# Performance work log

Hardware: AMD Instinct MI355X
Metric: run time of the kernel (lower is better)

Reference implementation:

```python
import jax, jax.numpy as jnp
import numpy as np

K_VALUES = (2, 4, 8)  # sorted k_values from init


def setup_inputs() -> dict:
    key = jax.random.key(0)
    ks = jax.random.split(key, 6)
    B, T, D, H = 16, 2048, 512, 64
    nk = len(K_VALUES)
    # columns: (E, Pt, eta, phi) -- E,Pt positive, eta in [-3,3], phi in [-pi,pi]
    u = jax.random.uniform(ks[0], (B, T, 4), jnp.float32)
    tokens_cont = u * jnp.array([100.0, 50.0, 6.0, 6.2832], jnp.float32) + jnp.array([1.0, 1.0, -3.0, -3.1416], jnp.float32)
    lengths = jax.random.randint(ks[1], (B,), T // 2, T + 1)
    mask = jnp.arange(T)[None, :] < lengths[:, None]  # [B,T] True=valid
    W1 = jax.random.normal(ks[2], (nk, H), jnp.float32) / np.sqrt(nk).astype(np.float32)
    b1 = jax.random.normal(ks[3], (H,), jnp.float32) * 0.01
    W2 = jax.random.normal(ks[4], (H, D), jnp.float32) / np.sqrt(H).astype(np.float32)
    b2 = jax.random.normal(ks[5], (D,), jnp.float32) * 0.01
    return dict(tokens_cont=tokens_cont, mask=mask, W1=W1, b1=b1, W2=W2, b2=b2)


def reference(tokens_cont, mask, W1, b1, W2, b2):
    B, T, _ = tokens_cont.shape
    E, Pt, eta, phi = (tokens_cont[..., i] for i in range(4))
    px = Pt * jnp.cos(phi)
    py = Pt * jnp.sin(phi)
    pz = Pt * jnp.sinh(jnp.clip(eta, -20.0, 20.0))
    P = jnp.stack([E, px, py, pz], axis=-1)  # [B,T,4] four-momentum
    metric = jnp.array([1.0, -1.0, -1.0, -1.0], P.dtype)
    # Lorentz dot: E_i E_j - px_i px_j - py_i py_j - pz_i pz_j -> [B,T,T]
    dot = jnp.einsum('btc,bsc->bts', P * metric, P)
    dot = jnp.where(mask[:, None, :], dot, -jnp.inf)  # exclude padding friends
    max_k = min(max(K_VALUES), T)
    _, topk_idx = jax.lax.top_k(dot, max_k)  # [B,T,max_k]
    Pf = P[jnp.arange(B)[:, None, None], topk_idx]  # gather friends [B,T,max_k,4]
    cum = jnp.cumsum(Pf, axis=2)  # prefix sums over sorted friends
    masses = []
    maskf = mask.astype(P.dtype)
    for k in K_VALUES:
        ps = cum[:, :, min(k, max_k) - 1, :]  # [B,T,4] summed 4-momentum of top-k group
        m2 = ps[..., 0] ** 2 - jnp.sum(ps[..., 1:] ** 2, axis=-1)
        m2 = jnp.maximum(m2, 0.0) * maskf
        masses.append(jnp.sqrt(m2 + 1e-8))
    mass = jnp.stack(masses, axis=-1)  # [B,T,n_k]
    h = jax.nn.gelu(mass @ W1 + b1, approximate=False)  # torch GELU = exact erf
    return h @ W2 + b2  # [B,T,model_dim]
```

## Files before the change

### kernel.cpp

```cpp
#include <hip/hip_runtime.h>
#include <hip/hip_bf16.h>
#include <math.h>

#define NB 16
#define NT 2048
#define ND 512
#define NH 64

typedef __attribute__((ext_vector_type(8))) short short8;
typedef __attribute__((ext_vector_type(4))) float float4v;

__device__ __forceinline__ bool mask_is_bytes(const int* m) {
    return m[0] == 0x01010101;
}
__device__ __forceinline__ bool mask_at(const int* m, bool bytes, int i) {
    if (bytes) return ((const unsigned char*)m)[i] != 0;
    return m[i] != 0;
}

__device__ __forceinline__ float dot4(float4 a, float4 p) {
    float d = a.x * p.x;
    d = __builtin_fmaf(a.y, p.y, d);
    d = __builtin_fmaf(a.z, p.z, d);
    d = __builtin_fmaf(a.w, p.w, d);
    return d;
}

__device__ __forceinline__ unsigned short f2bf(float x) {
    unsigned int u = __float_as_uint(x);
    u += 0x7fffu + ((u >> 16) & 1u);
    return (unsigned short)(u >> 16);
}

#define INS8(V0,V1,V2,V3,V4,V5,V6,V7,D)                          \
    {                                                            \
        float n0 = fmaxf(V0, D);                                 \
        float n1 = __builtin_amdgcn_fmed3f(D, V0, V1);           \
        float n2 = __builtin_amdgcn_fmed3f(D, V1, V2);           \
        float n3 = __builtin_amdgcn_fmed3f(D, V2, V3);           \
        float n4 = __builtin_amdgcn_fmed3f(D, V3, V4);           \
        float n5 = __builtin_amdgcn_fmed3f(D, V4, V5);           \
        float n6 = __builtin_amdgcn_fmed3f(D, V5, V6);           \
        float n7 = __builtin_amdgcn_fmed3f(D, V6, V7);           \
        V0 = n0; V1 = n1; V2 = n2; V3 = n3;                      \
        V4 = n4; V5 = n5; V6 = n6; V7 = n7;                      \
    }

__global__ void __launch_bounds__(256) w2t_kernel(
        const float* __restrict__ W2, unsigned short* __restrict__ W2t) {
    int i = blockIdx.x * 256 + threadIdx.x;
    int n = i & (ND - 1), k = i >> 9;
    W2t[n * NH + k] = f2bf(W2[k * ND + n]);
}

#define VT(w2, j, l)  scratch[((w2) * 8 + (j)) * 128 + (l)]
#define PS(w2, c, l)  scratch[((w2) * 12 + (c)) * 128 + (l)]

__global__ void __launch_bounds__(512) fused_topk_mass_mlp_kernel(
        const float* __restrict__ tok,
        const int* __restrict__ mask,
        const float* __restrict__ W1,
        const float* __restrict__ b1,
        const unsigned short* __restrict__ W2t,
        const float* __restrict__ b2,
        float* __restrict__ out) {
    __shared__ float Plds[NT * 4];
    __shared__ float scratch[8 * 12 * 128];
    __shared__ unsigned short hs[64][88];
    __shared__ float mass_s[3][128];
    __shared__ int wcnt[8];

    const int b    = blockIdx.y;
    const int t0   = blockIdx.x * 128;
    const int tid  = threadIdx.x;
    const int lane = tid & 63;
    const int w    = tid >> 6;
    const bool mb  = mask_is_bytes(mask);

    const bool blockValid = mask_at(mask, mb, b * NT + t0);

    if (blockValid) {
        int cnt = 0;
#pragma unroll
        for (int it = 0; it < 4; ++it) {
            int i = tid + it * 512;
            float4 tv = ((const float4*)tok)[b * NT + i];
            bool m = mask_at(mask, mb, b * NT + i);
            float E = tv.x, Pt = tv.y, eta = tv.z, phi = tv.w;
            float px = Pt * cosf(phi);
            float py = Pt * sinf(phi);
            float pz = Pt * sinhf(fminf(fmaxf(eta, -20.f), 20.f));
            float4 pv = m ? make_float4(E, px, py, pz)
                          : make_float4(-1e30f, 0.f, 0.f, 0.f);
            *(float4*)&Plds[i * 4] = pv;
            cnt += (int)__popcll(__ballot(m));
        }
        if (lane == 0) wcnt[w] = cnt;
        __syncthreads();

        int L = 0;
#pragma unroll
        for (int j = 0; j < 8; ++j) L += wcnt[j];
        const int C    = (L + 7) >> 3;
        const int sBeg = w * C;
        const int sEnd = min(sBeg + C, L);

        float4 ptA = *(const float4*)&Plds[(t0 + lane) * 4];
        float4 ptB = *(const float4*)&Plds[(t0 + 64 + lane) * 4];
        float4 aA  = make_float4(ptA.x, -ptA.y, -ptA.z, -ptA.w);
        float4 aB  = make_float4(ptB.x, -ptB.y, -ptB.z, -ptB.w);

        const float NEGBIG = -3.402823466e38f;
        float A0 = NEGBIG, A1 = NEGBIG, A2 = NEGBIG, A3 = NEGBIG;
        float A4 = NEGBIG, A5 = NEGBIG, A6 = NEGBIG, A7 = NEGBIG;
        float B0 = NEGBIG, B1 = NEGBIG, B2 = NEGBIG, B3 = NEGBIG;
        float B4 = NEGBIG, B5 = NEGBIG, B6 = NEGBIG, B7 = NEGBIG;

#pragma unroll 4
        for (int s = sBeg; s < sEnd; ++s) {
            float4 ps = *(const float4*)&Plds[s * 4];
            float dA = dot4(aA, ps);
            float dB = dot4(aB, ps);
            INS8(A0, A1, A2, A3, A4, A5, A6, A7, dA);
            INS8(B0, B1, B2, B3, B4, B5, B6, B7, dB);
        }
        VT(w, 0, lane) = A0; VT(w, 1, lane) = A1;
        VT(w, 2, lane) = A2; VT(w, 3, lane) = A3;
        VT(w, 4, lane) = A4; VT(w, 5, lane) = A5;
        VT(w, 6, lane) = A6; VT(w, 7, lane) = A7;
        VT(w, 0, 64 + lane) = B0; VT(w, 1, 64 + lane) = B1;
        VT(w, 2, 64 + lane) = B2; VT(w, 3, 64 + lane) = B3;
        VT(w, 4, 64 + lane) = B4; VT(w, 5, 64 + lane) = B5;
        VT(w, 6, 64 + lane) = B6; VT(w, 7, 64 + lane) = B7;
        __syncthreads();

        float mA0 = NEGBIG, mA1 = NEGBIG, mA2 = NEGBIG, mA3 = NEGBIG;
        float mA4 = NEGBIG, mA5 = NEGBIG, mA6 = NEGBIG, mA7 = NEGBIG;
        float mB0 = NEGBIG, mB1 = NEGBIG, mB2 = NEGBIG, mB3 = NEGBIG;
        float mB4 = NEGBIG, mB5 = NEGBIG, mB6 = NEGBIG, mB7 = NEGBIG;
#pragma unroll
        for (int w2 = 0; w2 < 8; ++w2) {
#pragma unroll
            for (int j = 0; j < 8; ++j) {
                float dA = VT(w2, j, lane);
                float dB = VT(w2, j, 64 + lane);
                INS8(mA0, mA1, mA2, mA3, mA4, mA5, mA6, mA7, dA);
                INS8(mB0, mB1, mB2, mB3, mB4, mB5, mB6, mB7, dB);
            }
        }
        const float th2A = mA1, th4A = mA3, th8A = mA7;
        const float th2B = mB1, th4B = mB3, th8B = mB7;
        __syncthreads();

        float a2x = 0.f, a2y = 0.f, a2z = 0.f, a2w = 0.f;
        float a4x = 0.f, a4y = 0.f, a4z = 0.f, a4w = 0.f;
        float a8x = 0.f, a8y = 0.f, a8z = 0.f, a8w = 0.f;
        float b2x = 0.f, b2y = 0.f, b2z = 0.f, b2w = 0.f;
        float b4x = 0.f, b4y = 0.f, b4z = 0.f, b4w = 0.f;
        float b8x = 0.f, b8y = 0.f, b8z = 0.f, b8w = 0.f;
#pragma unroll 4
        for (int s = sBeg; s < sEnd; ++s) {
            float4 ps = *(const float4*)&Plds[s * 4];
            float dA = dot4(aA, ps);
            float dB = dot4(aB, ps);
            if (dA >= th8A) {
                a8x += ps.x; a8y += ps.y; a8z += ps.z; a8w += ps.w;
                if (dA >= th4A) {
                    a4x += ps.x; a4y += ps.y; a4z += ps.z; a4w += ps.w;
                    if (dA >= th2A) {
                        a2x += ps.x; a2y += ps.y; a2z += ps.z; a2w += ps.w;
                    }
                }
            }
            if (dB >= th8B) {
                b8x += ps.x; b8y += ps.y; b8z += ps.z; b8w += ps.w;
                if (dB >= th4B) {
                    b4x += ps.x; b4y += ps.y; b4z += ps.z; b4w += ps.w;
                    if (dB >= th2B) {
                        b2x += ps.x; b2y += ps.y; b2z += ps.z; b2w += ps.w;
                    }
                }
            }
        }
        PS(w, 0, lane) = a2x;  PS(w, 1, lane) = a2y;
        PS(w, 2, lane) = a2z;  PS(w, 3, lane) = a2w;
        PS(w, 4, lane) = a4x;  PS(w, 5, lane) = a4y;
        PS(w, 6, lane) = a4z;  PS(w, 7, lane) = a4w;
        PS(w, 8, lane) = a8x;  PS(w, 9, lane) = a8y;
        PS(w, 10, lane) = a8z; PS(w, 11, lane) = a8w;
        PS(w, 0, 64 + lane) = b2x;  PS(w, 1, 64 + lane) = b2y;
        PS(w, 2, 64 + lane) = b2z;  PS(w, 3, 64 + lane) = b2w;
        PS(w, 4, 64 + lane) = b4x;  PS(w, 5, 64 + lane) = b4y;
        PS(w, 6, 64 + lane) = b4z;  PS(w, 7, 64 + lane) = b4w;
        PS(w, 8, 64 + lane) = b8x;  PS(w, 9, 64 + lane) = b8y;
        PS(w, 10, 64 + lane) = b8z; PS(w, 11, 64 + lane) = b8w;
        __syncthreads();

        if (w < 2) {
            const int tl = w * 64 + lane;
            float tot[12];
#pragma unroll
            for (int c = 0; c < 12; ++c) {
                float acc = 0.f;
#pragma unroll
                for (int w2 = 0; w2 < 8; ++w2) acc += PS(w2, c, tl);
                tot[c] = acc;
            }
            const bool maskt = (t0 + tl) < L;
            const float MZ = sqrtf(1e-8f);
            auto massf = [&](float sx, float sy, float sz, float sw) -> float {
                float q = sx * sx;
                q = __builtin_fmaf(-sy, sy, q);
                q = __builtin_fmaf(-sz, sz, q);
                q = __builtin_fmaf(-sw, sw, q);
                q = fmaxf(q, 0.f);
                return sqrtf(q + 1e-8f);
            };
            mass_s[0][tl] = maskt ? massf(tot[0], tot[1], tot[2], tot[3]) : MZ;
            mass_s[1][tl] = maskt ? massf(tot[4], tot[5], tot[6], tot[7]) : MZ;
            mass_s[2][tl] = maskt ? massf(tot[8], tot[9], tot[10], tot[11]) : MZ;
        }
    } else {
        if (tid < 128) {
            const float MZ = sqrtf(1e-8f);
            mass_s[0][tid] = MZ;
            mass_s[1][tid] = MZ;
            mass_s[2][tid] = MZ;
        }
    }
    __syncthreads();

    const int col   = lane & 15;
    const int quad  = lane >> 4;
    const int mhalf = w >> 2;
    const int nBase = (w & 3) * 128;

#pragma unroll
    for (int half = 0; half < 2; ++half) {
        {
            const int tt = lane;
            const int hr = w;
            float q0 = mass_s[0][half * 64 + tt];
            float q1 = mass_s[1][half * 64 + tt];
            float q2 = mass_s[2][half * 64 + tt];
            unsigned short hv[8];
#pragma unroll
            for (int j = 0; j < 8; ++j) {
                int hh = hr * 8 + j;
                float pre = b1[hh];
                pre = __builtin_fmaf(q0, W1[hh], pre);
                pre = __builtin_fmaf(q1, W1[NH + hh], pre);
                pre = __builtin_fmaf(q2, W1[2 * NH + hh], pre);
                float g = 0.5f * pre * (1.0f + erff(pre * 0.70710678118654752f));
                hv[j] = f2bf(g);
            }
            *(short8*)&hs[tt][hr * 8] = *(const short8*)hv;
        }
        __syncthreads();

        short8 afrag[2][2];
#pragma unroll
        for (int mt = 0; mt < 2; ++mt)
#pragma unroll
            for (int ks = 0; ks < 2; ++ks)
                afrag[mt][ks] = *(const short8*)&hs[mhalf * 32 + mt * 16 + col][ks * 32 + quad * 8];

        float4v acc[2][8];
#pragma unroll
        for (int mt = 0; mt < 2; ++mt)
#pragma unroll
            for (int nt = 0; nt < 8; ++nt)
                acc[mt][nt] = (float4v)(0.f);

#pragma unroll
        for (int nt = 0; nt < 8; ++nt) {
            const unsigned short* wp = W2t + (nBase + nt * 16 + col) * NH + quad * 8;
            short8 bf0 = *(const short8*)(wp);
            short8 bf1 = *(const short8*)(wp + 32);
            acc[0][nt] = __builtin_amdgcn_mfma_f32_16x16x32_bf16(afrag[0][0], bf0, acc[0][nt], 0, 0, 0);
            acc[1][nt] = __builtin_amdgcn_mfma_f32_16x16x32_bf16(afrag[1][0], bf0, acc[1][nt], 0, 0, 0);
            acc[0][nt] = __builtin_amdgcn_mfma_f32_16x16x32_bf16(afrag[0][1], bf1, acc[0][nt], 0, 0, 0);
            acc[1][nt] = __builtin_amdgcn_mfma_f32_16x16x32_bf16(afrag[1][1], bf1, acc[1][nt], 0, 0, 0);
        }

#pragma unroll
        for (int nt = 0; nt < 8; ++nt) {
            float bias = b2[nBase + nt * 16 + col];
#pragma unroll
            for (int mt = 0; mt < 2; ++mt) {
                int mRow = b * NT + t0 + half * 64 + mhalf * 32 + mt * 16 + quad * 4;
                size_t base = (size_t)mRow * ND + nBase + nt * 16 + col;
#pragma unroll
                for (int r = 0; r < 4; ++r) {
                    out[base + (size_t)r * ND] = acc[mt][nt][r] + bias;
                }
            }
        }
        __syncthreads();
    }
}

extern "C" void kernel_launch(void* const* d_in, const int* in_sizes, int n_in,
                              void* d_out, int out_size, void* d_ws, size_t ws_size,
                              hipStream_t stream) {
    const float* tok  = (const float*)d_in[0];
    const int*   mask = (const int*)d_in[1];
    const float* W1   = (const float*)d_in[2];
    const float* b1   = (const float*)d_in[3];
    const float* W2   = (const float*)d_in[4];
    const float* b2   = (const float*)d_in[5];
    float*       out  = (float*)d_out;

    unsigned short* W2t = (unsigned short*)d_ws;

    w2t_kernel<<<dim3(ND * NH / 256), dim3(256), 0, stream>>>(W2, W2t);

    dim3 gB(NT / 128, NB);
    fused_topk_mass_mlp_kernel<<<gB, dim3(512), 0, stream>>>(
        tok, mask, W1, b1, W2t, b2, out);
}
```

Baseline: 148.7 us.

## Double block to 1024 threads, skip top-8 inserts via wave ballot, single-pass MLP

Raises the fused kernel to 16 waves per block so each wave scans half as many candidate friends. The 16 partial top-8 lists are merged, and the partial momentum sums are reduced in two steps through the same scratch buffer. The expensive 8-wide insertion network is now skipped whenever no lane in the wave has a candidate beating its current 8th-best. The MLP epilogue runs once over all 128 rows instead of two halves. Register pressure from launch_bounds(1024) may cause spills, and the larger scratch and hs arrays use more LDS.

```diff
diff --git a/kernel.cpp b/kernel.cpp
--- a/kernel.cpp
+++ b/kernel.cpp
@@ -56,7 +56,7 @@
 #define VT(w2, j, l)  scratch[((w2) * 8 + (j)) * 128 + (l)]
 #define PS(w2, c, l)  scratch[((w2) * 12 + (c)) * 128 + (l)]
 
-__global__ void __launch_bounds__(512) fused_topk_mass_mlp_kernel(
+__global__ void __launch_bounds__(1024, 4) fused_topk_mass_mlp_kernel(
         const float* __restrict__ tok,
         const int* __restrict__ mask,
         const float* __restrict__ W1,
@@ -65,10 +65,10 @@
         const float* __restrict__ b2,
         float* __restrict__ out) {
     __shared__ float Plds[NT * 4];
-    __shared__ float scratch[8 * 12 * 128];
-    __shared__ unsigned short hs[64][88];
+    __shared__ float scratch[16 * 8 * 128];
+    __shared__ unsigned short hs[128][88];
     __shared__ float mass_s[3][128];
-    __shared__ int wcnt[8];
+    __shared__ int wcnt[16];
 
     const int b    = blockIdx.y;
     const int t0   = blockIdx.x * 128;
@@ -82,8 +82,8 @@
     if (blockValid) {
         int cnt = 0;
 #pragma unroll
-        for (int it = 0; it < 4; ++it) {
-            int i = tid + it * 512;
+        for (int it = 0; it < 2; ++it) {
+            int i = tid + it * 1024;
             float4 tv = ((const float4*)tok)[b * NT + i];
             bool m = mask_at(mask, mb, b * NT + i);
             float E = tv.x, Pt = tv.y, eta = tv.z, phi = tv.w;
@@ -100,8 +100,8 @@
 
         int L = 0;
 #pragma unroll
-        for (int j = 0; j < 8; ++j) L += wcnt[j];
-        const int C    = (L + 7) >> 3;
+        for (int j = 0; j < 16; ++j) L += wcnt[j];
+        const int C    = (L + 15) >> 4;
         const int sBeg = w * C;
         const int sEnd = min(sBeg + C, L);
 
@@ -116,13 +116,14 @@
         float B0 = NEGBIG, B1 = NEGBIG, B2 = NEGBIG, B3 = NEGBIG;
         float B4 = NEGBIG, B5 = NEGBIG, B6 = NEGBIG, B7 = NEGBIG;
 
-#pragma unroll 4
         for (int s = sBeg; s < sEnd; ++s) {
             float4 ps = *(const float4*)&Plds[s * 4];
             float dA = dot4(aA, ps);
             float dB = dot4(aB, ps);
-            INS8(A0, A1, A2, A3, A4, A5, A6, A7, dA);
-            INS8(B0, B1, B2, B3, B4, B5, B6, B7, dB);
+            if (__ballot((dA > A7) || (dB > B7))) {
+                INS8(A0, A1, A2, A3, A4, A5, A6, A7, dA);
+                INS8(B0, B1, B2, B3, B4, B5, B6, B7, dB);
+            }
         }
         VT(w, 0, lane) = A0; VT(w, 1, lane) = A1;
         VT(w, 2, lane) = A2; VT(w, 3, lane) = A3;
@@ -139,7 +140,7 @@
         float mB0 = NEGBIG, mB1 = NEGBIG, mB2 = NEGBIG, mB3 = NEGBIG;
         float mB4 = NEGBIG, mB5 = NEGBIG, mB6 = NEGBIG, mB7 = NEGBIG;
 #pragma unroll
-        for (int w2 = 0; w2 < 8; ++w2) {
+        for (int w2 = 0; w2 < 16; ++w2) {
 #pragma unroll
             for (int j = 0; j < 8; ++j) {
                 float dA = VT(w2, j, lane);
@@ -155,10 +156,9 @@
         float a2x = 0.f, a2y = 0.f, a2z = 0.f, a2w = 0.f;
         float a4x = 0.f, a4y = 0.f, a4z = 0.f, a4w = 0.f;
         float a8x = 0.f, a8y = 0.f, a8z = 0.f, a8w = 0.f;
-        float b2x = 0.f, b2y = 0.f, b2z = 0.f, b2w = 0.f;
-        float b4x = 0.f, b4y = 0.f, b4z = 0.f, b4w = 0.f;
-        float b8x = 0.f, b8y = 0.f, b8z = 0.f, b8w = 0.f;
-#pragma unroll 4
+        float c2x = 0.f, c2y = 0.f, c2z = 0.f, c2w = 0.f;
+        float c4x = 0.f, c4y = 0.f, c4z = 0.f, c4w = 0.f;
+        float c8x = 0.f, c8y = 0.f, c8z = 0.f, c8w = 0.f;
         for (int s = sBeg; s < sEnd; ++s) {
             float4 ps = *(const float4*)&Plds[s * 4];
             float dA = dot4(aA, ps);
@@ -173,27 +173,46 @@
                 }
             }
             if (dB >= th8B) {
-                b8x += ps.x; b8y += ps.y; b8z += ps.z; b8w += ps.w;
+                c8x += ps.x; c8y += ps.y; c8z += ps.z; c8w += ps.w;
                 if (dB >= th4B) {
-                    b4x += ps.x; b4y += ps.y; b4z += ps.z; b4w += ps.w;
+                    c4x += ps.x; c4y += ps.y; c4z += ps.z; c4w += ps.w;
                     if (dB >= th2B) {
-                        b2x += ps.x; b2y += ps.y; b2z += ps.z; b2w += ps.w;
+                        c2x += ps.x; c2y += ps.y; c2z += ps.z; c2w += ps.w;
                     }
                 }
             }
         }
-        PS(w, 0, lane) = a2x;  PS(w, 1, lane) = a2y;
-        PS(w, 2, lane) = a2z;  PS(w, 3, lane) = a2w;
-        PS(w, 4, lane) = a4x;  PS(w, 5, lane) = a4y;
-        PS(w, 6, lane) = a4z;  PS(w, 7, lane) = a4w;
-        PS(w, 8, lane) = a8x;  PS(w, 9, lane) = a8y;
-        PS(w, 10, lane) = a8z; PS(w, 11, lane) = a8w;
-        PS(w, 0, 64 + lane) = b2x;  PS(w, 1, 64 + lane) = b2y;
-        PS(w, 2, 64 + lane) = b2z;  PS(w, 3, 64 + lane) = b2w;
-        PS(w, 4, 64 + lane) = b4x;  PS(w, 5, 64 + lane) = b4y;
-        PS(w, 6, 64 + lane) = b4z;  PS(w, 7, 64 + lane) = b4w;
-        PS(w, 8, 64 + lane) = b8x;  PS(w, 9, 64 + lane) = b8y;
-        PS(w, 10, 64 + lane) = b8z; PS(w, 11, 64 + lane) = b8w;
+
+        if (w >= 8) {
+            const int ws = w - 8;
+            PS(ws, 0, lane) = a2x;  PS(ws, 1, lane) = a2y;
+            PS(ws, 2, lane) = a2z;  PS(ws, 3, lane) = a2w;
+            PS(ws, 4, lane) = a4x;  PS(ws, 5, lane) = a4y;
+            PS(ws, 6, lane) = a4z;  PS(ws, 7, lane) = a4w;
+            PS(ws, 8, lane) = a8x;  PS(ws, 9, lane) = a8y;
+            PS(ws, 10, lane) = a8z; PS(ws, 11, lane) = a8w;
+            PS(ws, 0, 64 + lane) = c2x;  PS(ws, 1, 64 + lane) = c2y;
+            PS(ws, 2, 64 + lane) = c2z;  PS(ws, 3, 64 + lane) = c2w;
+            PS(ws, 4, 64 + lane) = c4x;  PS(ws, 5, 64 + lane) = c4y;
+            PS(ws, 6, 64 + lane) = c4z;  PS(ws, 7, 64 + lane) = c4w;
+            PS(ws, 8, 64 + lane) = c8x;  PS(ws, 9, 64 + lane) = c8y;
+            PS(ws, 10, 64 + lane) = c8z; PS(ws, 11, 64 + lane) = c8w;
+        }
+        __syncthreads();
+        if (w < 8) {
+            PS(w, 0, lane) += a2x;  PS(w, 1, lane) += a2y;
+            PS(w, 2, lane) += a2z;  PS(w, 3, lane) += a2w;
+            PS(w, 4, lane) += a4x;  PS(w, 5, lane) += a4y;
+            PS(w, 6, lane) += a4z;  PS(w, 7, lane) += a4w;
+            PS(w, 8, lane) += a8x;  PS(w, 9, lane) += a8y;
+            PS(w, 10, lane) += a8z; PS(w, 11, lane) += a8w;
+            PS(w, 0, 64 + lane) += c2x;  PS(w, 1, 64 + lane) += c2y;
+            PS(w, 2, 64 + lane) += c2z;  PS(w, 3, 64 + lane) += c2w;
+            PS(w, 4, 64 + lane) += c4x;  PS(w, 5, 64 + lane) += c4y;
+            PS(w, 6, 64 + lane) += c4z;  PS(w, 7, 64 + lane) += c4w;
+            PS(w, 8, 64 + lane) += c8x;  PS(w, 9, 64 + lane) += c8y;
+            PS(w, 10, 64 + lane) += c8z; PS(w, 11, 64 + lane) += c8w;
+        }
         __syncthreads();
 
         if (w < 2) {
@@ -230,73 +249,69 @@
     }
     __syncthreads();
 
-    const int col   = lane & 15;
-    const int quad  = lane >> 4;
-    const int mhalf = w >> 2;
-    const int nBase = (w & 3) * 128;
-
-#pragma unroll
-    for (int half = 0; half < 2; ++half) {
-        {
-            const int tt = lane;
-            const int hr = w;
-            float q0 = mass_s[0][half * 64 + tt];
-            float q1 = mass_s[1][half * 64 + tt];
-            float q2 = mass_s[2][half * 64 + tt];
-            unsigned short hv[8];
-#pragma unroll
-            for (int j = 0; j < 8; ++j) {
-                int hh = hr * 8 + j;
-                float pre = b1[hh];
-                pre = __builtin_fmaf(q0, W1[hh], pre);
-                pre = __builtin_fmaf(q1, W1[NH + hh], pre);
-                pre = __builtin_fmaf(q2, W1[2 * NH + hh], pre);
-                float g = 0.5f * pre * (1.0f + erff(pre * 0.70710678118654752f));
-                hv[j] = f2bf(g);
-            }
-            *(short8*)&hs[tt][hr * 8] = *(const short8*)hv;
-        }
-        __syncthreads();
-
-        short8 afrag[2][2];
-#pragma unroll
-        for (int mt = 0; mt < 2; ++mt)
-#pragma unroll
-            for (int ks = 0; ks < 2; ++ks)
-                afrag[mt][ks] = *(const short8*)&hs[mhalf * 32 + mt * 16 + col][ks * 32 + quad * 8];
-
-        float4v acc[2][8];
-#pragma unroll
-        for (int mt = 0; mt < 2; ++mt)
-#pragma unroll
-            for (int nt = 0; nt < 8; ++nt)
-                acc[mt][nt] = (float4v)(0.f);
-
-#pragma unroll
-        for (int nt = 0; nt < 8; ++nt) {
-            const unsigned short* wp = W2t + (nBase + nt * 16 + col) * NH + quad * 8;
-            short8 bf0 = *(const short8*)(wp);
-            short8 bf1 = *(const short8*)(wp + 32);
-            acc[0][nt] = __builtin_amdgcn_mfma_f32_16x16x32_bf16(afrag[0][0], bf0, acc[0][nt], 0, 0, 0);
-            acc[1][nt] = __builtin_amdgcn_mfma_f32_16x16x32_bf16(afrag[1][0], bf0, acc[1][nt], 0, 0, 0);
-            acc[0][nt] = __builtin_amdgcn_mfma_f32_16x16x32_bf16(afrag[0][1], bf1, acc[0][nt], 0, 0, 0);
-            acc[1][nt] = __builtin_amdgcn_mfma_f32_16x16x32_bf16(afrag[1][1], bf1, acc[1][nt], 0, 0, 0);
-        }
-
-#pragma unroll
-        for (int nt = 0; nt < 8; ++nt) {
-            float bias = b2[nBase + nt * 16 + col];
-#pragma unroll
-            for (int mt = 0; mt < 2; ++mt) {
-                int mRow = b * NT + t0 + half * 64 + mhalf * 32 + mt * 16 + quad * 4;
-                size_t base = (size_t)mRow * ND + nBase + nt * 16 + col;
-#pragma unroll
-                for (int r = 0; r < 4; ++r) {
-                    out[base + (size_t)r * ND] = acc[mt][nt][r] + bias;
-                }
-            }
-        }
-        __syncthreads();
+    {
+        const int tt = tid & 127;
+        const int hr = tid >> 7;
+        float q0 = mass_s[0][tt];
+        float q1 = mass_s[1][tt];
+        float q2 = mass_s[2][tt];
+        unsigned short hv[8];
+#pragma unroll
+        for (int j = 0; j < 8; ++j) {
+            int hh = hr * 8 + j;
+            float pre = b1[hh];
+            pre = __builtin_fmaf(q0, W1[hh], pre);
+            pre = __builtin_fmaf(q1, W1[NH + hh], pre);
+            pre = __builtin_fmaf(q2, W1[2 * NH + hh], pre);
+            float g = 0.5f * pre * (1.0f + erff(pre * 0.70710678118654752f));
+            hv[j] = f2bf(g);
+        }
+        *(short8*)&hs[tt][hr * 8] = *(const short8*)hv;
+    }
+    __syncthreads();
+
+    const int col    = lane & 15;
+    const int quad   = lane >> 4;
+    const int mslice = w >> 2;
+    const int nBase  = (w & 3) * 128;
+
+    short8 afrag[2][2];
+#pragma unroll
+    for (int mt = 0; mt < 2; ++mt)
+#pragma unroll
+        for (int ks = 0; ks < 2; ++ks)
+            afrag[mt][ks] = *(const short8*)&hs[mslice * 32 + mt * 16 + col][ks * 32 + quad * 8];
+
+    float4v acc[2][8];
+#pragma unroll
+    for (int mt = 0; mt < 2; ++mt)
+#pragma unroll
+        for (int nt = 0; nt < 8; ++nt)
+            acc[mt][nt] = (float4v)(0.f);
+
+#pragma unroll
+    for (int nt = 0; nt < 8; ++nt) {
+        const unsigned short* wp = W2t + (nBase + nt * 16 + col) * NH + quad * 8;
+        short8 bf0 = *(const short8*)(wp);
+        short8 bf1 = *(const short8*)(wp + 32);
+        acc[0][nt] = __builtin_amdgcn_mfma_f32_16x16x32_bf16(afrag[0][0], bf0, acc[0][nt], 0, 0, 0);
+        acc[1][nt] = __builtin_amdgcn_mfma_f32_16x16x32_bf16(afrag[1][0], bf0, acc[1][nt], 0, 0, 0);
+        acc[0][nt] = __builtin_amdgcn_mfma_f32_16x16x32_bf16(afrag[0][1], bf1, acc[0][nt], 0, 0, 0);
+        acc[1][nt] = __builtin_amdgcn_mfma_f32_16x16x32_bf16(afrag[1][1], bf1, acc[1][nt], 0, 0, 0);
+    }
+
+#pragma unroll
+    for (int nt = 0; nt < 8; ++nt) {
+        float bias = b2[nBase + nt * 16 + col];
+#pragma unroll
+        for (int mt = 0; mt < 2; ++mt) {
+            int mRow = b * NT + t0 + mslice * 32 + mt * 16 + quad * 4;
+            size_t base = (size_t)mRow * ND + nBase + nt * 16 + col;
+#pragma unroll
+            for (int r = 0; r < 4; ++r) {
+                out[base + (size_t)r * ND] = acc[mt][nt][r] + bias;
+            }
+        }
     }
 }
 
@@ -316,6 +331,6 @@
     w2t_kernel<<<dim3(ND * NH / 256), dim3(256), 0, stream>>>(W2, W2t);
 
     dim3 gB(NT / 128, NB);
-    fused_topk_mass_mlp_kernel<<<gB, dim3(512), 0, stream>>>(
+    fused_topk_mass_mlp_kernel<<<gB, dim3(1024), 0, stream>>>(
         tok, mask, W1, b1, W2t, b2, out);
 }
```

Measured after the change: 191.4 us. 1.29x slower.
